# Optimization experiments

Measured on AMD Instinct MI355X. Metric: run time of the kernel, lower is better.

## Reference

```python
import jax, jax.numpy as jnp
import numpy as np
from jax.scipy.special import ndtr, logsumexp

K = 2  # top-k experts (init kwarg k=2)


def setup_inputs() -> dict:
    key = jax.random.key(0)
    k1, k2, k3, k4 = jax.random.split(key, 4)
    B, D, E = 131072, 1024, 64
    x_flat = jax.random.normal(k1, (B, D), jnp.float32)
    # Original inits w_gate/w_noise to zeros; use small random weights so
    # top-k routing is non-degenerate for correctness testing.
    w_gate = jax.random.normal(k2, (D, E), jnp.float32) * 0.02
    w_noise = jax.random.normal(k3, (D, E), jnp.float32) * 0.02
    eps = jax.random.normal(k4, (B, E), jnp.float32)  # reified torch.randn_like
    return {"x_flat": x_flat, "w_gate": w_gate, "w_noise": w_noise, "eps": eps}


def _cv_squared(v):
    # torch .var() is unbiased (ddof=1)
    return jnp.var(v, ddof=1) / (jnp.mean(v) ** 2 + 1e-10)


def reference(x_flat, w_gate, w_noise, eps):
    B = x_flat.shape[0]
    clean_logits = x_flat @ w_gate                                  # [B, E]
    noise_stddev = jax.nn.softplus(x_flat @ w_noise) + 0.01         # [B, E]
    logits = clean_logits + eps * noise_stddev                      # noisy logits (training)

    top_vals, top_idx = jax.lax.top_k(logits, K + 1)                # [B, K+1], sorted desc
    top_k_gates = jax.nn.softmax(top_vals[:, :K], axis=-1)          # [B, K]
    gates = jnp.zeros_like(logits).at[jnp.arange(B)[:, None], top_idx[:, :K]].set(top_k_gates)

    # _prob_in_top_k load estimate (noisy gating, k < num_experts, training)
    thr_if_in = top_vals[:, K:K + 1]                                # (k+1)-th largest
    thr_if_out = top_vals[:, K - 1:K]                               # k-th largest
    is_in = logits > thr_if_in
    prob_if_in = ndtr((clean_logits - thr_if_in) / noise_stddev)
    prob_if_out = ndtr((clean_logits - thr_if_out) / noise_stddev)
    load = jnp.where(is_in, prob_if_in, prob_if_out).sum(0)         # [E]

    importance = gates.sum(0)                                       # [E]
    z_loss = logsumexp(logits, axis=-1).mean()                      # log(sum(exp)).mean()
    load_balancing = _cv_squared(importance) + _cv_squared(load) + z_loss
    return gates, load, logits, load_balancing, importance
```

## Files before the change

### kernel.cpp

```cpp
#include <hip/hip_runtime.h>
#include <math.h>

#define B_ROWS 131072
#define D_DIM  1024
#define E_EXP  64
#define MARGIN 4e-3f

typedef _Float16 f16;
typedef _Float16 f16x8 __attribute__((ext_vector_type(8)));
typedef float    f32x4 __attribute__((ext_vector_type(4)));

#define AS1C(p) ((const __attribute__((address_space(1))) void*)(p))
#define AS3(p)  ((__attribute__((address_space(3))) void*)(p))


__device__ __forceinline__ float softplus_f(float t) {
  return (t > 20.0f) ? t : log1pf(expf(t));
}
__device__ __forceinline__ float ndtr_f(float z) {
  return 0.5f * erfcf(-z * 0.70710678118654752f);
}
__device__ __forceinline__ void argmax64(float& v, int& vi) {
  #pragma unroll
  for (int off = 32; off > 0; off >>= 1) {
    float ov = __shfl_xor(v, off, 64);
    int   oi = __shfl_xor(vi, off, 64);
    if (ov > v || (ov == v && oi < vi)) { v = ov; vi = oi; }
  }
}
__device__ __forceinline__ float sum64(float v) {
  #pragma unroll
  for (int off = 32; off > 0; off >>= 1) v += __shfl_xor(v, off, 64);
  return v;
}

__device__ __forceinline__ void row_epilogue_exact(
    int row, int lane, float clean, float sd, float l,
    float* __restrict__ gates_buf, float* __restrict__ logits_buf,
    float& load_acc, float& imp_acc, float& z_acc)
{
  float v1 = l; int i1 = lane; argmax64(v1, i1);
  float v2 = (lane == i1) ? -INFINITY : l; int i2 = lane; argmax64(v2, i2);
  float v3 = (lane == i1 || lane == i2) ? -INFINITY : l; int i3 = lane; argmax64(v3, i3);
  (void)i3;
  const float e21 = expf(v2 - v1);
  const float g1  = 1.0f / (1.0f + e21);
  const float g2  = e21 * g1;
  const float gv  = (lane == i1) ? g1 : ((lane == i2) ? g2 : 0.0f);
  gates_buf [(size_t)row * E_EXP + lane] = gv;
  logits_buf[(size_t)row * E_EXP + lane] = l;
  const float ssum = sum64(expf(l - v1));
  z_acc += v1 + logf(ssum);
  const float thr = (l > v3) ? v3 : v2;
  load_acc += ndtr_f((clean - thr) / sd);
  imp_acc  += gv;
}


__global__ __launch_bounds__(256) void prep_wt(
    const float* __restrict__ wg, const float* __restrict__ wn, f16* __restrict__ wt,
    float* load_o, float* imp_o, float* zsum, int* flagcnt) {
  if (blockIdx.x == 0) {
    const int t = threadIdx.x;
    if (t < 64) { load_o[t] = 0.0f; imp_o[t] = 0.0f; }
    if (t == 64) zsum[0] = 0.0f;
    if (t == 65) flagcnt[0] = 0;
  }
  __shared__ float tile[64][65];
  const int m  = blockIdx.x >> 4;
  const int kt = blockIdx.x & 15;
  const int k0 = kt * 64;
  const float* src = m ? wn : wg;
  const int c = threadIdx.x & 63;
  const int r0 = threadIdx.x >> 6;
  #pragma unroll
  for (int r = r0; r < 64; r += 4)
    tile[r][c] = src[(size_t)(k0 + r) * 64 + c];
  __syncthreads();
  const int j = threadIdx.x & 63;
  #pragma unroll
  for (int col = r0; col < 64; col += 4)
    wt[(size_t)(m * 64 + col) * 1024 + k0 + j] = (f16)tile[j][col];
}

__global__ __launch_bounds__(256, 3) void gemm_fused(
    const float* __restrict__ x, const f16* __restrict__ wt,
    const float* __restrict__ eps,
    float* __restrict__ gates_buf, float* __restrict__ logits_buf,
    float* __restrict__ load_o, float* __restrict__ imp_o, float* __restrict__ zsum,
    int* __restrict__ flagcnt, int* __restrict__ flaglist)
{
  __shared__ __align__(16) char wlds[2][16384];

  const int tid  = threadIdx.x;
  const int lane = tid & 63;
  const int wid  = tid >> 6;
  const int l15  = lane & 15;
  const int l4   = lane >> 4;
  const size_t rowbase = (size_t)blockIdx.x * 128 + wid * 32;

  const int scol0 = wid * 8 + (lane >> 3);
  const int skel  = ((lane & 7) * 8) ^ ((lane >> 3) << 3);
  const f16* wsrc0 = wt + (size_t)(scol0 +  0) * 1024 + skel;
  const f16* wsrc1 = wt + (size_t)(scol0 + 32) * 1024 + skel;
  const f16* wsrc2 = wt + (size_t)(scol0 + 64) * 1024 + skel;
  const f16* wsrc3 = wt + (size_t)(scol0 + 96) * 1024 + skel;

#define ISSUE_B(buf, kc) do {                                                                      \
    __builtin_amdgcn_global_load_lds(AS1C(wsrc0 + (kc) * 64), AS3(&wlds[buf][0*4096 + wid*1024]), 16, 0, 0); \
    __builtin_amdgcn_global_load_lds(AS1C(wsrc1 + (kc) * 64), AS3(&wlds[buf][1*4096 + wid*1024]), 16, 0, 0); \
    __builtin_amdgcn_global_load_lds(AS1C(wsrc2 + (kc) * 64), AS3(&wlds[buf][2*4096 + wid*1024]), 16, 0, 0); \
    __builtin_amdgcn_global_load_lds(AS1C(wsrc3 + (kc) * 64), AS3(&wlds[buf][3*4096 + wid*1024]), 16, 0, 0); \
  } while (0)

#define PIPE_BARRIER() do {                                  \
    asm volatile("s_waitcnt vmcnt(8)" ::: "memory");         \
    __builtin_amdgcn_s_barrier();                            \
    __builtin_amdgcn_sched_barrier(0);                       \
  } while (0)

  const float* xp0 = x + (rowbase +  0 + l15) * D_DIM + l4 * 8;
  const float* xp1 = x + (rowbase + 16 + l15) * D_DIM + l4 * 8;

  f32x4 acc[2][8];
  #pragma unroll
  for (int rt = 0; rt < 2; ++rt)
    #pragma unroll
    for (int et = 0; et < 8; ++et) acc[rt][et] = (f32x4)0.0f;

  float4 xa[8];
#define LOAD_A(kc) do {                                                  \
    _Pragma("unroll")                                                    \
    for (int kl = 0; kl < 2; ++kl) {                                     \
      xa[kl*4 + 0] = *(const float4*)(xp0 + (kc)*64 + kl*32 + 0);        \
      xa[kl*4 + 1] = *(const float4*)(xp0 + (kc)*64 + kl*32 + 4);        \
      xa[kl*4 + 2] = *(const float4*)(xp1 + (kc)*64 + kl*32 + 0);        \
      xa[kl*4 + 3] = *(const float4*)(xp1 + (kc)*64 + kl*32 + 4);        \
    }                                                                    \
  } while (0)

  ISSUE_B(0, 0);
  LOAD_A(0);
  PIPE_BARRIER();

  #pragma unroll 1
  for (int kc = 0; kc < 16; ++kc) {
    const int buf = kc & 1;

    if (kc < 15) ISSUE_B(buf ^ 1, kc + 1);

    f16x8 af[2][2];
    #pragma unroll
    for (int kl = 0; kl < 2; ++kl)
      #pragma unroll
      for (int rt = 0; rt < 2; ++rt) {
        #pragma unroll
        for (int h = 0; h < 2; ++h) {
          const float4 v = xa[kl*4 + rt*2 + h];
          af[kl][rt][h*4 + 0] = (f16)v.x;
          af[kl][rt][h*4 + 1] = (f16)v.y;
          af[kl][rt][h*4 + 2] = (f16)v.z;
          af[kl][rt][h*4 + 3] = (f16)v.w;
        }
      }

    if (kc < 15) LOAD_A(kc + 1);

    #pragma unroll
    for (int kl = 0; kl < 2; ++kl) {
      #pragma unroll
      for (int et = 0; et < 8; ++et) {
        const int bcol = et * 16 + l15;
        const int boff = (bcol * 128 + kl * 64 + l4 * 16) ^ ((l15 & 7) << 4);
        const f16x8 b = *(const f16x8*)(&wlds[buf][boff]);
        acc[0][et] = __builtin_amdgcn_mfma_f32_16x16x32_f16(af[kl][0], b, acc[0][et], 0, 0, 0);
        acc[1][et] = __builtin_amdgcn_mfma_f32_16x16x32_f16(af[kl][1], b, acc[1][et], 0, 0, 0);
      }
    }

    if (kc < 15) PIPE_BARRIER();
  }
#undef ISSUE_B
#undef LOAD_A
#undef PIPE_BARRIER

  float load_acc[4] = {0.f, 0.f, 0.f, 0.f};
  float imp_acc[4]  = {0.f, 0.f, 0.f, 0.f};
  float z_acc = 0.f;

  #pragma unroll
  for (int rt = 0; rt < 2; ++rt) {
    #pragma unroll
    for (int rg = 0; rg < 4; ++rg) {
      const size_t row = rowbase + rt * 16 + l4 * 4 + rg;
      float cl[4], sd[4], lg[4];
      #pragma unroll
      for (int j = 0; j < 4; ++j) {
        cl[j] = acc[rt][j][rg];
        sd[j] = softplus_f(acc[rt][4 + j][rg]) + 0.01f;
        const float ev = eps[row * E_EXP + j * 16 + l15];
        lg[j] = fmaf(ev, sd[j], cl[j]);
      }
      float v = lg[0]; int c = l15;
      #pragma unroll
      for (int j = 1; j < 4; ++j) {
        const int cj = j * 16 + l15;
        if (lg[j] > v || (lg[j] == v && cj < c)) { v = lg[j]; c = cj; }
      }
      #pragma unroll
      for (int off = 1; off < 16; off <<= 1) {
        const float ov = __shfl_xor(v, off, 64);
        const int   oc = __shfl_xor(c, off, 64);
        if (ov > v || (ov == v && oc < c)) { v = ov; c = oc; }
      }
      const float v1 = v; const int i1 = c;
      v = -INFINITY; c = 1 << 30;
      #pragma unroll
      for (int j = 0; j < 4; ++j) {
        const int cj = j * 16 + l15;
        if (cj != i1 && (lg[j] > v || (lg[j] == v && cj < c))) { v = lg[j]; c = cj; }
      }
      #pragma unroll
      for (int off = 1; off < 16; off <<= 1) {
        const float ov = __shfl_xor(v, off, 64);
        const int   oc = __shfl_xor(c, off, 64);
        if (ov > v || (ov == v && oc < c)) { v = ov; c = oc; }
      }
      const float v2 = v; const int i2 = c;
      float v3 = -INFINITY;
      #pragma unroll
      for (int j = 0; j < 4; ++j) {
        const int cj = j * 16 + l15;
        if (cj != i1 && cj != i2) v3 = fmaxf(v3, lg[j]);
      }
      #pragma unroll
      for (int off = 1; off < 16; off <<= 1) v3 = fmaxf(v3, __shfl_xor(v3, off, 64));

      if (v2 - v3 >= MARGIN) {
        const float e21 = expf(v2 - v1);
        const float g1  = 1.0f / (1.0f + e21);
        const float g2  = e21 * g1;
        float s = 0.f;
        #pragma unroll
        for (int j = 0; j < 4; ++j) s += expf(lg[j] - v1);
        #pragma unroll
        for (int off = 1; off < 16; off <<= 1) s += __shfl_xor(s, off, 64);
        if (l15 == 0) z_acc += v1 + logf(s);
        #pragma unroll
        for (int j = 0; j < 4; ++j) {
          const int cj = j * 16 + l15;
          const float gv = (cj == i1) ? g1 : ((cj == i2) ? g2 : 0.0f);
          gates_buf [row * E_EXP + cj] = gv;
          logits_buf[row * E_EXP + cj] = lg[j];
          imp_acc[j] += gv;
          const float thr = (lg[j] > v3) ? v3 : v2;
          load_acc[j] += ndtr_f((cl[j] - thr) / sd[j]);
        }
      } else {
        if (l15 == 0) { const int idx = atomicAdd(flagcnt, 1); flaglist[idx] = (int)row; }
      }
    }
  }

  float* red = (float*)&wlds[0][0];
  #pragma unroll
  for (int j = 0; j < 4; ++j) {
    float L = load_acc[j]; L += __shfl_xor(L, 16, 64); L += __shfl_xor(L, 32, 64);
    float I = imp_acc[j];  I += __shfl_xor(I, 16, 64); I += __shfl_xor(I, 32, 64);
    if (l4 == 0) {
      red[wid * 64 + j * 16 + l15]       = L;
      red[256 + wid * 64 + j * 16 + l15] = I;
    }
  }
  {
    const float zw = sum64(z_acc);
    if (lane == 0) red[512 + wid] = zw;
  }
  __syncthreads();
  if (wid == 0) {
    const float L = red[lane] + red[64 + lane] + red[128 + lane] + red[192 + lane];
    const float I = red[256 + lane] + red[320 + lane] + red[384 + lane] + red[448 + lane];
    atomicAdd(&load_o[lane], L);
    atomicAdd(&imp_o[lane],  I);
    if (lane == 0) atomicAdd(zsum, red[512] + red[513] + red[514] + red[515]);
  }
}

__global__ __launch_bounds__(256) void fixup_k(
    const float* __restrict__ x, const float* __restrict__ wg, const float* __restrict__ wn,
    const float* __restrict__ eps,
    float* __restrict__ gates_buf, float* __restrict__ logits_buf,
    float* __restrict__ load_o, float* __restrict__ imp_o, float* __restrict__ zsum,
    const int* __restrict__ flagcnt, const int* __restrict__ flaglist)
{
  const int lane = threadIdx.x & 63;
  const int wid  = threadIdx.x >> 6;
  __shared__ float redg[4][4][64], redn[4][4][64];

  const int nf = *flagcnt;

  for (int it = blockIdx.x * 4; it < nf; it += gridDim.x * 4) {
    const int nr = (nf - it < 4) ? (nf - it) : 4;
    int rows[4];
    #pragma unroll
    for (int rr = 0; rr < 4; ++rr) rows[rr] = flaglist[it + ((rr < nr) ? rr : 0)];

    float dg[4] = {0.f,0.f,0.f,0.f}, dn[4] = {0.f,0.f,0.f,0.f};
    const int dbase = wid * 256;
    for (int d = 0; d < 256; d += 4) {
      const int db = (dbase + d) * E_EXP + lane;
      const float wgv0 = wg[db], wgv1 = wg[db + 64], wgv2 = wg[db + 128], wgv3 = wg[db + 192];
      const float wnv0 = wn[db], wnv1 = wn[db + 64], wnv2 = wn[db + 128], wnv3 = wn[db + 192];
      #pragma unroll
      for (int rr = 0; rr < 4; ++rr) {
        const float4 xv = *(const float4*)(x + (size_t)rows[rr] * D_DIM + dbase + d);
        dg[rr] = fmaf(xv.x, wgv0, dg[rr]);  dn[rr] = fmaf(xv.x, wnv0, dn[rr]);
        dg[rr] = fmaf(xv.y, wgv1, dg[rr]);  dn[rr] = fmaf(xv.y, wnv1, dn[rr]);
        dg[rr] = fmaf(xv.z, wgv2, dg[rr]);  dn[rr] = fmaf(xv.z, wnv2, dn[rr]);
        dg[rr] = fmaf(xv.w, wgv3, dg[rr]);  dn[rr] = fmaf(xv.w, wnv3, dn[rr]);
      }
    }
    #pragma unroll
    for (int rr = 0; rr < 4; ++rr) { redg[wid][rr][lane] = dg[rr]; redn[wid][rr][lane] = dn[rr]; }
    __syncthreads();
    if (wid < nr) {
      const int row = rows[wid];
      const float clean = redg[0][wid][lane] + redg[1][wid][lane] + redg[2][wid][lane] + redg[3][wid][lane];
      const float sdraw = redn[0][wid][lane] + redn[1][wid][lane] + redn[2][wid][lane] + redn[3][wid][lane];
      const float sd = softplus_f(sdraw) + 0.01f;
      const float ev = eps[(size_t)row * E_EXP + lane];
      const float l  = fmaf(ev, sd, clean);
      float la = 0.f, ia = 0.f, za = 0.f;
      row_epilogue_exact(row, lane, clean, sd, l, gates_buf, logits_buf, la, ia, za);
      atomicAdd(&load_o[lane], la);
      atomicAdd(&imp_o[lane],  ia);
      if (lane == 0) atomicAdd(zsum, za);
    }
    __syncthreads();
  }
}

__global__ void finalize_k(const float* __restrict__ load_o,
                           const float* __restrict__ imp_o,
                           const float* __restrict__ zsum,
                           float* __restrict__ out_lb) {
  const int e = threadIdx.x & 63;
  const double a = (double)load_o[e];
  const double b = (double)imp_o[e];
  double sl = a, sl2 = a * a, si = b, si2 = b * b;
  #pragma unroll
  for (int off = 32; off > 0; off >>= 1) {
    sl  += __shfl_xor(sl,  off, 64);
    sl2 += __shfl_xor(sl2, off, 64);
    si  += __shfl_xor(si,  off, 64);
    si2 += __shfl_xor(si2, off, 64);
  }
  if (e == 0) {
    const double n  = (double)E_EXP;
    const double ml = sl / n, mi = si / n;
    const double varl = (sl2 - n * ml * ml) / (n - 1.0);
    const double vari = (si2 - n * mi * mi) / (n - 1.0);
    const double cvl = varl / (ml * ml + 1e-10);
    const double cvi = vari / (mi * mi + 1e-10);
    const double z  = (double)zsum[0] / (double)B_ROWS;
    out_lb[0] = (float)(cvi + cvl + z);
  }
}


extern "C" void kernel_launch(void* const* d_in, const int* in_sizes, int n_in,
                              void* d_out, int out_size, void* d_ws, size_t ws_size,
                              hipStream_t stream) {
  const float* x   = (const float*)d_in[0];
  const float* wg  = (const float*)d_in[1];
  const float* wn  = (const float*)d_in[2];
  const float* eps = (const float*)d_in[3];

  float* out    = (float*)d_out;
  float* gates  = out;
  float* load_o = out + (size_t)B_ROWS * E_EXP;
  float* logits = load_o + E_EXP;
  float* lb     = logits + (size_t)B_ROWS * E_EXP;
  float* imp    = lb + 1;

  float* zsum     = (float*)d_ws;
  int*   flagcnt  = (int*)d_ws + 2;
  int*   flaglist = (int*)((char*)d_ws + 256);
  f16*   wt       = (f16*)((char*)d_ws + 256 + 4 * (size_t)B_ROWS);

  prep_wt<<<32, 256, 0, stream>>>(wg, wn, wt, load_o, imp, zsum, flagcnt);
  gemm_fused<<<B_ROWS / 128, 256, 0, stream>>>(
      x, wt, eps, gates, logits, load_o, imp, zsum, flagcnt, flaglist);
  fixup_k<<<512, 256, 0, stream>>>(x, wg, wn, eps, gates, logits, load_o, imp, zsum, flagcnt, flaglist);
  finalize_k<<<1, 64, 0, stream>>>(load_o, imp, zsum, lb);
}
```

Baseline: 274.0 us.

## Triple-buffer weight tiles in LDS and double-buffer converted activation fragments

The weight-tile LDS ring grows from two to three buffers, so each weight tile is issued two K-steps ahead. Activation loads are prefetched two steps ahead, and the fp16 conversion of the next step runs before the current step's MFMAs, using two register fragment sets. The K loop is fully unrolled and the explicit vmcnt wait is removed, which leaves memory-counter waits to the compiler. The aim is to hide global load latency behind MFMA work, at the cost of more LDS (48KB per block), more registers, and possibly conservative compiler-inserted waits; a barrier is added before the LDS reduction reuses the buffer.

```diff
diff --git a/kernel.cpp b/kernel.cpp
--- a/kernel.cpp
+++ b/kernel.cpp
@@ -90,7 +90,7 @@
     float* __restrict__ load_o, float* __restrict__ imp_o, float* __restrict__ zsum,
     int* __restrict__ flagcnt, int* __restrict__ flaglist)
 {
-  __shared__ __align__(16) char wlds[2][16384];
+  __shared__ __align__(16) char wlds[3][16384];
 
   const int tid  = threadIdx.x;
   const int lane = tid & 63;
@@ -106,15 +106,15 @@
   const f16* wsrc2 = wt + (size_t)(scol0 + 64) * 1024 + skel;
   const f16* wsrc3 = wt + (size_t)(scol0 + 96) * 1024 + skel;
 
-#define ISSUE_B(buf, kc) do {                                                                      \
-    __builtin_amdgcn_global_load_lds(AS1C(wsrc0 + (kc) * 64), AS3(&wlds[buf][0*4096 + wid*1024]), 16, 0, 0); \
-    __builtin_amdgcn_global_load_lds(AS1C(wsrc1 + (kc) * 64), AS3(&wlds[buf][1*4096 + wid*1024]), 16, 0, 0); \
-    __builtin_amdgcn_global_load_lds(AS1C(wsrc2 + (kc) * 64), AS3(&wlds[buf][2*4096 + wid*1024]), 16, 0, 0); \
-    __builtin_amdgcn_global_load_lds(AS1C(wsrc3 + (kc) * 64), AS3(&wlds[buf][3*4096 + wid*1024]), 16, 0, 0); \
+#define ISSUE_B(bufc, kc) do {                                                                        \
+    __builtin_amdgcn_global_load_lds(AS1C(wsrc0 + (kc) * 64), AS3(&wlds[bufc][0*4096 + wid*1024]), 16, 0, 0); \
+    __builtin_amdgcn_global_load_lds(AS1C(wsrc1 + (kc) * 64), AS3(&wlds[bufc][1*4096 + wid*1024]), 16, 0, 0); \
+    __builtin_amdgcn_global_load_lds(AS1C(wsrc2 + (kc) * 64), AS3(&wlds[bufc][2*4096 + wid*1024]), 16, 0, 0); \
+    __builtin_amdgcn_global_load_lds(AS1C(wsrc3 + (kc) * 64), AS3(&wlds[bufc][3*4096 + wid*1024]), 16, 0, 0); \
   } while (0)
 
 #define PIPE_BARRIER() do {                                  \
-    asm volatile("s_waitcnt vmcnt(8)" ::: "memory");         \
+    __builtin_amdgcn_sched_barrier(0);                       \
     __builtin_amdgcn_s_barrier();                            \
     __builtin_amdgcn_sched_barrier(0);                       \
   } while (0)
@@ -139,32 +139,40 @@
     }                                                                    \
   } while (0)
 
+  f16x8 af[2][2][2];
+#define CVT(par) do {                                                    \
+    _Pragma("unroll")                                                    \
+    for (int kl = 0; kl < 2; ++kl)                                       \
+      _Pragma("unroll")                                                  \
+      for (int rt = 0; rt < 2; ++rt) {                                   \
+        _Pragma("unroll")                                                \
+        for (int h = 0; h < 2; ++h) {                                    \
+          const float4 v = xa[kl*4 + rt*2 + h];                          \
+          af[par][kl][rt][h*4 + 0] = (f16)v.x;                           \
+          af[par][kl][rt][h*4 + 1] = (f16)v.y;                           \
+          af[par][kl][rt][h*4 + 2] = (f16)v.z;                           \
+          af[par][kl][rt][h*4 + 3] = (f16)v.w;                           \
+        }                                                                \
+      }                                                                  \
+  } while (0)
+
   ISSUE_B(0, 0);
+  ISSUE_B(1, 1);
   LOAD_A(0);
+  CVT(0);
+  __builtin_amdgcn_sched_barrier(0);
+  LOAD_A(1);
   PIPE_BARRIER();
 
-  #pragma unroll 1
+  #pragma unroll
   for (int kc = 0; kc < 16; ++kc) {
-    const int buf = kc & 1;
-
-    if (kc < 15) ISSUE_B(buf ^ 1, kc + 1);
-
-    f16x8 af[2][2];
-    #pragma unroll
-    for (int kl = 0; kl < 2; ++kl)
-      #pragma unroll
-      for (int rt = 0; rt < 2; ++rt) {
-        #pragma unroll
-        for (int h = 0; h < 2; ++h) {
-          const float4 v = xa[kl*4 + rt*2 + h];
-          af[kl][rt][h*4 + 0] = (f16)v.x;
-          af[kl][rt][h*4 + 1] = (f16)v.y;
-          af[kl][rt][h*4 + 2] = (f16)v.z;
-          af[kl][rt][h*4 + 3] = (f16)v.w;
-        }
-      }
-
-    if (kc < 15) LOAD_A(kc + 1);
+    if (kc + 2 < 16) ISSUE_B((kc + 2) % 3, kc + 2);
+
+    if (kc + 1 < 16) {
+      CVT((kc + 1) & 1);
+      __builtin_amdgcn_sched_barrier(0);
+      LOAD_A(kc + 2 < 16 ? kc + 2 : 0);
+    }
 
     #pragma unroll
     for (int kl = 0; kl < 2; ++kl) {
@@ -172,9 +180,9 @@
       for (int et = 0; et < 8; ++et) {
         const int bcol = et * 16 + l15;
         const int boff = (bcol * 128 + kl * 64 + l4 * 16) ^ ((l15 & 7) << 4);
-        const f16x8 b = *(const f16x8*)(&wlds[buf][boff]);
-        acc[0][et] = __builtin_amdgcn_mfma_f32_16x16x32_f16(af[kl][0], b, acc[0][et], 0, 0, 0);
-        acc[1][et] = __builtin_amdgcn_mfma_f32_16x16x32_f16(af[kl][1], b, acc[1][et], 0, 0, 0);
+        const f16x8 b = *(const f16x8*)(&wlds[kc % 3][boff]);
+        acc[0][et] = __builtin_amdgcn_mfma_f32_16x16x32_f16(af[kc & 1][kl][0], b, acc[0][et], 0, 0, 0);
+        acc[1][et] = __builtin_amdgcn_mfma_f32_16x16x32_f16(af[kc & 1][kl][1], b, acc[1][et], 0, 0, 0);
       }
     }
 
@@ -182,6 +190,7 @@
   }
 #undef ISSUE_B
 #undef LOAD_A
+#undef CVT
 #undef PIPE_BARRIER
 
   float load_acc[4] = {0.f, 0.f, 0.f, 0.f};
@@ -262,6 +271,7 @@
     }
   }
 
+  __syncthreads();
   float* red = (float*)&wlds[0][0];
   #pragma unroll
   for (int j = 0; j < 4; ++j) {
```

Result: slower. 295.5 us (+7.8%).
